# Performance work log

Measured on AMD Instinct MI355X. Metric: run time of the kernel, lower is better.

The kernel has to match this reference:

```python
import jax, jax.numpy as jnp
import numpy as np

N_NODES = 100_000
N_EDGES = 1_600_000
IN_FEATS = 64
H_DIMS = 64
OUT_A = 2
OUT_B = 21
N_LAYERS = 2
EPS = 1e-5


def setup_inputs() -> dict:
    key = jax.random.key(0)
    ks = jax.random.split(key, 16)
    d = H_DIMS

    def rn(k, shape, scale=0.05):
        return jax.random.normal(k, shape, dtype=jnp.float32) * scale

    return {
        "v": jax.random.normal(ks[0], (N_NODES, IN_FEATS), dtype=jnp.float32),
        "src": jax.random.randint(ks[1], (N_EDGES,), 0, N_NODES),
        "dst": jax.random.randint(ks[2], (N_EDGES,), 0, N_NODES),
        "rel_type": jax.random.randint(ks[3], (N_EDGES,), 0, 3),
        "norm": jax.random.uniform(ks[4], (N_EDGES,), dtype=jnp.float32),
        "emb_W": rn(ks[5], (d, IN_FEATS)),
        "emb_b": jnp.zeros((d,), jnp.float32),
        "emb_gamma": jnp.ones((d,), jnp.float32),
        "emb_beta": jnp.zeros((d,), jnp.float32),
        "rel_weight": rn(ks[6], (3, d, d)),
        "gru_Wih": rn(ks[7], (3 * d, d)),
        "gru_Whh": rn(ks[8], (3 * d, d)),
        "gru_bih": jnp.zeros((3 * d,), jnp.float32),
        "gru_bhh": jnp.zeros((3 * d,), jnp.float32),
        "ker_gamma": jnp.ones((d,), jnp.float32),
        "ker_beta": jnp.zeros((d,), jnp.float32),
        "a_W1": rn(ks[9], (d, d)), "a_b1": jnp.zeros((d,), jnp.float32),
        "a_gamma": jnp.ones((d,), jnp.float32), "a_beta": jnp.zeros((d,), jnp.float32),
        "a_W2": rn(ks[10], (OUT_A, d)), "a_b2": jnp.zeros((OUT_A,), jnp.float32),
        "b_W1": rn(ks[11], (d, d)), "b_b1": jnp.zeros((d,), jnp.float32),
        "b_gamma": jnp.ones((d,), jnp.float32), "b_beta": jnp.zeros((d,), jnp.float32),
        "b_W2": rn(ks[12], (OUT_B, d)), "b_b2": jnp.zeros((OUT_B,), jnp.float32),
    }


def _bn(x, gamma, beta):
    # BatchNorm1d in training mode: batch statistics, biased variance
    mu = jnp.mean(x, axis=0)
    var = jnp.var(x, axis=0)
    return (x - mu) * jax.lax.rsqrt(var + EPS) * gamma + beta


def _gru_cell(x, h, Wih, Whh, bih, bhh):
    # torch nn.GRU single layer, gate order (r, z, n)
    gi = x @ Wih.T + bih
    gh = h @ Whh.T + bhh
    ir, iz, inn = jnp.split(gi, 3, axis=-1)
    hr, hz, hn = jnp.split(gh, 3, axis=-1)
    r = jax.nn.sigmoid(ir + hr)
    z = jax.nn.sigmoid(iz + hz)
    n = jnp.tanh(inn + r * hn)
    return (1.0 - z) * n + z * h


def reference(v, src, dst, rel_type, norm, emb_W, emb_b, emb_gamma, emb_beta,
              rel_weight, gru_Wih, gru_Whh, gru_bih, gru_bhh, ker_gamma, ker_beta,
              a_W1, a_b1, a_gamma, a_beta, a_W2, a_b2,
              b_W1, b_b1, b_gamma, b_beta, b_W2, b_b2):
    # Embedding: Linear -> BN -> ReLU
    h0 = jax.nn.relu(_bn(v @ emb_W.T + emb_b, emb_gamma, emb_beta))
    output = h0
    h = jnp.zeros_like(h0)
    n_nodes = v.shape[0]
    for _ in range(N_LAYERS):
        # per-node relational transform for all 3 relations: [N, 3, d]
        x3 = jnp.einsum('nd,rdk->nrk', output, rel_weight)
        msg = x3[src, rel_type] * norm[:, None]                     # [E, d]
        swh = jax.ops.segment_sum(msg, dst, num_segments=n_nodes)   # [N, d]
        h = _gru_cell(swh, h, gru_Wih, gru_Whh, gru_bih, gru_bhh)
        output = h
    hk = _bn(output, ker_gamma, ker_beta)
    # task heads: Linear -> BN -> ReLU -> Linear (MLP with h_layers=2)
    xa = jax.nn.relu(_bn(hk @ a_W1.T + a_b1, a_gamma, a_beta)) @ a_W2.T + a_b2
    xb = jax.nn.relu(_bn(hk @ b_W1.T + b_b1, b_gamma, b_beta)) @ b_W2.T + b_b2
    return xa, xb
```

## Files before the change

### kernel.cpp

```cpp
#include <hip/hip_runtime.h>

#define NN 100000
#define NE 1600000
#define NP 100096
#define NBKT 391
#define CAP 6144
#define EPSV 1e-5f

typedef unsigned int u32;
typedef unsigned short u16;
typedef unsigned long long u64;
typedef __bf16 bf16x8 __attribute__((ext_vector_type(8)));
typedef float f32x4 __attribute__((ext_vector_type(4)));

#define GLBP(x) ((const __attribute__((address_space(1))) u32*)(x))
#define LDSP(x) ((__attribute__((address_space(3))) u32*)(x))

__device__ __forceinline__ u16 f2bf(float f) {
  u32 x = __float_as_uint(f);
  return (u16)((x + 0x7FFFu + ((x >> 16) & 1u)) >> 16);
}
__device__ __forceinline__ float bf2f(u16 h) { return __uint_as_float(((u32)h) << 16); }

__device__ __forceinline__ void pack_one(const float* W, u32* out, int K, int KOT, int i) {
  int q = i & 3, lane = (i >> 2) & 63, f = i >> 8;
  int ks = f / KOT, ot = f - ks * KOT;
  int o = ot * 16 + (lane & 15);
  int k = ks * 32 + (lane >> 4) * 8 + q * 2;
  out[i] = (u32)f2bf(W[o * K + k]) | ((u32)f2bf(W[o * K + k + 1]) << 16);
}

__global__ void setupA(const float* __restrict__ relw, const float* __restrict__ Wih,
                       const float* __restrict__ embW, const float* __restrict__ Whh,
                       float* __restrict__ Wrow, u32* __restrict__ PWem, u32* __restrict__ PWhh) {
  int b = blockIdx.x;
  if (b < 144) {
    int t = b * 256 + threadIdx.x;
    if (t >= 192 * 192) return;
    int kg = t / 192, j = t % 192;
    const float* a = relw + (j >> 6) * 4096 + (j & 63) * 64;
    const float* w = Wih + kg * 64;
    float s = 0.f;
#pragma unroll
    for (int k = 0; k < 64; ++k) s += a[k] * w[k];
    Wrow[kg * 192 + j] = s;
  } else if (b < 152) {
    pack_one(embW, PWem, 64, 4, (b - 144) * 256 + threadIdx.x);
  } else {
    pack_one(Whh, PWhh, 64, 12, (b - 152) * 256 + threadIdx.x);
  }
}

__global__ void pack_wf(const float* __restrict__ Wrow, u32* __restrict__ PWf) {
  pack_one(Wrow, PWf, 192, 12, blockIdx.x * 256 + threadIdx.x);
}

__global__ void fold_pack(const float* __restrict__ Wa, const float* __restrict__ Wb,
                          const float* __restrict__ sc, u32* __restrict__ Pa,
                          u32* __restrict__ Pb) {
  int iu = blockIdx.x * 256 + threadIdx.x;
  int hsel = iu >> 11;
  int i = iu & 2047;
  const float* W = hsel ? Wb : Wa;
  u32* P = hsel ? Pb : Pa;
  int q = i & 3, lane = (i >> 2) & 63, f = i >> 8;
  int ks = f >> 2, ot = f & 3;
  int o = ot * 16 + (lane & 15);
  int k = ks * 32 + (lane >> 4) * 8 + q * 2;
  P[i] = (u32)f2bf(W[o * 64 + k] * sc[k]) | ((u32)f2bf(W[o * 64 + k + 1] * sc[k + 1]) << 16);
}

__global__ __launch_bounds__(256) void countplace(const int* __restrict__ src,
                                                  const int* __restrict__ dst,
                                                  const int* __restrict__ rt,
                                                  const float* __restrict__ nrm,
                                                  int* __restrict__ gcnt,
                                                  u64* __restrict__ region) {
  __shared__ u32 hist[NBKT], gbase[NBKT];
  const int t = threadIdx.x;
  for (int i = t; i < NBKT; i += 256) hist[i] = 0;
  __syncthreads();
  const int e0 = blockIdx.x * 2048 + t;
  u32 rlo[8], rhi[8], lrank[8];
  int bkt[8];
#pragma unroll
  for (int i = 0; i < 8; ++i) {
    int e = e0 + i * 256;
    bkt[i] = -1;
    if (e < NE) {
      int d = dst[e];
      int b = d >> 8;
      bkt[i] = b;
      lrank[i] = atomicAdd(&hist[b], 1u);
      rlo[i] = (u32)src[e] | ((u32)rt[e] << 20) | ((u32)(d & 255) << 22);
      rhi[i] = __float_as_uint(nrm[e]);
    }
  }
  __syncthreads();
  for (int i = t; i < NBKT; i += 256) {
    u32 h = hist[i];
    gbase[i] = h ? (u32)atomicAdd(&gcnt[i], (int)h) : 0u;
  }
  __syncthreads();
#pragma unroll
  for (int i = 0; i < 8; ++i) {
    if (bkt[i] >= 0) {
      u32 pos = gbase[bkt[i]] + lrank[i];
      if (pos < CAP)
        region[(size_t)bkt[i] * CAP + pos] = (u64)rlo[i] | ((u64)rhi[i] << 32);
    }
  }
}

__global__ __launch_bounds__(512) void bucketscan(const int* __restrict__ gcnt,
                                                  int* __restrict__ bbase,
                                                  int* __restrict__ rowp) {
  int t = threadIdx.x;
  int v = (t < NBKT) ? gcnt[t] : 0;
  __shared__ int sh[512];
  sh[t] = v;
  __syncthreads();
#pragma unroll
  for (int off = 1; off < 512; off <<= 1) {
    int u = (t >= off) ? sh[t - off] : 0;
    __syncthreads();
    sh[t] += u;
    __syncthreads();
  }
  if (t < NBKT) bbase[t] = sh[t] - v;
  if (t == 0) rowp[NN] = NE;
}

__global__ __launch_bounds__(256) void localsort(const int* __restrict__ gcnt,
                                                 const int* __restrict__ bbase,
                                                 const u64* __restrict__ region,
                                                 u64* __restrict__ csr,
                                                 int* __restrict__ rowp) {
  const int b = blockIdx.x, t = threadIdx.x;
  int n = gcnt[b];
  if (n > CAP) n = CAP;
  const int base = bbase[b];
  __shared__ u32 hist[256], sc[256];
  hist[t] = 0;
  __syncthreads();
  for (int i = t; i < n; i += 256)
    atomicAdd(&hist[((u32)region[(size_t)b * CAP + i] >> 22) & 255], 1u);
  __syncthreads();
  u32 v = hist[t];
  sc[t] = v;
  __syncthreads();
#pragma unroll
  for (int off = 1; off < 256; off <<= 1) {
    u32 u = (t >= off) ? sc[t - off] : 0;
    __syncthreads();
    sc[t] += u;
    __syncthreads();
  }
  u32 excl = sc[t] - v;
  int node = b * 256 + t;
  if (node < NN) rowp[node] = base + (int)excl;
  __syncthreads();
  hist[t] = excl;
  __syncthreads();
  for (int i = t; i < n; i += 256) {
    u64 rec = region[(size_t)b * CAP + i];
    u32 pos = atomicAdd(&hist[((u32)rec >> 22) & 255], 1u);
    csr[(size_t)base + pos] = rec;
  }
}

__global__ __launch_bounds__(256) void csr_gather(const int* __restrict__ rowp,
                                                  const u64* __restrict__ csr,
                                                  const u16* __restrict__ Xbf,
                                                  u16* __restrict__ ACCbf) {
  int wv = blockIdx.x * 4 + (threadIdx.x >> 6);
  int lane = threadIdx.x & 63;
  if (wv >= NN) return;
  const int half = lane >> 5, c2 = lane & 31;
  int base = rowp[wv], end = rowp[wv + 1];
  float a0x = 0.f, a0y = 0.f, a1x = 0.f, a1y = 0.f, a2x = 0.f, a2y = 0.f;
#define GP(JJ)                                                                   \
  { u32 sA = (u32)__builtin_amdgcn_readlane((int)lo, (JJ));                      \
    u32 sB = (u32)__builtin_amdgcn_readlane((int)lo, (JJ) + 1);                  \
    u32 nA = (u32)__builtin_amdgcn_readlane((int)hi, (JJ));                      \
    u32 nB = (u32)__builtin_amdgcn_readlane((int)hi, (JJ) + 1);                  \
    u32 srp = half ? sB : sA;                                                    \
    float nm = __uint_as_float(half ? nB : nA);                                  \
    u32 xw = *(const u32*)(Xbf + (size_t)(srp & 0xFFFFFu) * 64 + 2 * c2);        \
    float x0 = bf2f((u16)xw), x1 = bf2f((u16)(xw >> 16));                        \
    int r = (int)((srp >> 20) & 3);                                              \
    float n0 = (r == 0) ? nm : 0.f;                                              \
    float n1 = (r == 1) ? nm : 0.f;                                              \
    float n2 = (r == 2) ? nm : 0.f;                                              \
    a0x = fmaf(x0, n0, a0x); a0y = fmaf(x1, n0, a0y);                            \
    a1x = fmaf(x0, n1, a1x); a1y = fmaf(x1, n1, a1y);                            \
    a2x = fmaf(x0, n2, a2x); a2y = fmaf(x1, n2, a2y); }
  for (int c = base; c < end; c += 64) {
    int m = end - c; m = m > 64 ? 64 : m;
    u32 lo = 0, hi = 0;
    if (lane < m) {
      u64 r = csr[(size_t)c + lane];
      lo = (u32)r; hi = (u32)(r >> 32);
    }
    int j = 0;
    for (; j + 16 <= m; j += 16) {
      GP(j) GP(j + 2) GP(j + 4) GP(j + 6)
      GP(j + 8) GP(j + 10) GP(j + 12) GP(j + 14)
    }
    for (; j < m; j += 2) { GP(j) }
  }
#undef GP
  a0x += __shfl_xor(a0x, 32); a0y += __shfl_xor(a0y, 32);
  a1x += __shfl_xor(a1x, 32); a1y += __shfl_xor(a1y, 32);
  a2x += __shfl_xor(a2x, 32); a2y += __shfl_xor(a2y, 32);
  if (half == 0) {
    u32* orow = (u32*)(ACCbf + (size_t)wv * 192);
    orow[c2]      = (u32)f2bf(a0x) | ((u32)f2bf(a0y) << 16);
    orow[32 + c2] = (u32)f2bf(a1x) | ((u32)f2bf(a1y) << 16);
    orow[64 + c2] = (u32)f2bf(a2x) | ((u32)f2bf(a2y) << 16);
  }
}

template<int K, int KO, int AF32, int GRU, int CS, int OUTBF>
__global__ __launch_bounds__(256) void gemm_mfma(
    const void* __restrict__ Av, const u32* __restrict__ Wpk, void* __restrict__ Yv,
    const float* __restrict__ bih, const float* __restrict__ bhh,
    const u16* __restrict__ G2B, const u16* __restrict__ Hv,
    float* __restrict__ csum, int n) {
  constexpr int KOT = KO / 16, KS = K / 32;
  constexpr int NFRAG = KS * KOT;
  __shared__ u32 bsh[NFRAG * 256];
  __shared__ float cs[128];
  const int lane = threadIdx.x & 63, w = threadIdx.x >> 6;
  const int rr = lane & 15, kg = lane >> 4;
  const long mbase = (long)blockIdx.x * 128 + w * 32;
  const u16* Abf = (const u16*)Av;
  const float* Af = (const float*)Av;

  auto loadAbf = [&](int ks, int halfsel) -> bf16x8 {
    if (AF32) {
      long r = mbase + halfsel * 16 + rr;
      if (r > n - 1) r = n - 1;
      const float* pp = Af + r * K + ks * 32 + kg * 8;
      float4 u0 = *(const float4*)pp;
      float4 u1 = *(const float4*)(pp + 4);
      bf16x8 o_;
      o_[0] = __builtin_bit_cast(__bf16, f2bf(u0.x));
      o_[1] = __builtin_bit_cast(__bf16, f2bf(u0.y));
      o_[2] = __builtin_bit_cast(__bf16, f2bf(u0.z));
      o_[3] = __builtin_bit_cast(__bf16, f2bf(u0.w));
      o_[4] = __builtin_bit_cast(__bf16, f2bf(u1.x));
      o_[5] = __builtin_bit_cast(__bf16, f2bf(u1.y));
      o_[6] = __builtin_bit_cast(__bf16, f2bf(u1.z));
      o_[7] = __builtin_bit_cast(__bf16, f2bf(u1.w));
      return o_;
    }
    return *reinterpret_cast<const bf16x8*>(Abf + (mbase + halfsel * 16 + rr) * K + ks * 32 + kg * 8);
  };

  constexpr int PASSES = NFRAG / 4;
#pragma unroll
  for (int i = 0; i < PASSES; ++i) {
    int c = i * 4 + w;
    __builtin_amdgcn_global_load_lds(GLBP(Wpk + (long)c * 256 + lane * 4),
                                     LDSP(&bsh[c * 256]), 16, 0, 0);
  }
  bf16x8 a0 = loadAbf(0, 0);
  bf16x8 a1 = loadAbf(0, 1);
  __syncthreads();

  f32x4 acc[2][KOT] = {};
#pragma unroll
  for (int ks = 0; ks < KS; ++ks) {
    bf16x8 c0 = a0, c1 = a1;
    if (ks + 1 < KS) {
      a0 = loadAbf(ks + 1, 0);
      a1 = loadAbf(ks + 1, 1);
    }
#pragma unroll
    for (int o = 0; o < KOT; ++o) {
      bf16x8 bfr = *reinterpret_cast<const bf16x8*>(&bsh[((ks * KOT + o) * 64 + lane) * 4]);
      acc[0][o] = __builtin_amdgcn_mfma_f32_16x16x32_bf16(c0, bfr, acc[0][o], 0, 0, 0);
      acc[1][o] = __builtin_amdgcn_mfma_f32_16x16x32_bf16(c1, bfr, acc[1][o], 0, 0, 0);
    }
  }

  float s[4] = {0.f, 0.f, 0.f, 0.f}, ss[4] = {0.f, 0.f, 0.f, 0.f};
  if (GRU == 0) {
#pragma unroll
    for (int tl = 0; tl < 2; ++tl)
#pragma unroll
      for (int o = 0; o < KOT; ++o)
#pragma unroll
        for (int q = 0; q < 4; ++q) {
          long row = mbase + tl * 16 + kg * 4 + q;
          float vv = acc[tl][o][q];
          if (row < n) {
            long off = row * KO + o * 16 + rr;
            if (OUTBF) ((u16*)Yv)[off] = f2bf(vv);
            else       ((float*)Yv)[off] = vv;
            if (CS) { s[o & 3] += vv; ss[o & 3] += vv * vv; }
          }
        }
  } else {
    float bi[12], bh_[12];
#pragma unroll
    for (int g = 0; g < 3; ++g)
#pragma unroll
      for (int o = 0; o < 4; ++o) {
        bi[g * 4 + o] = bih[g * 64 + o * 16 + rr];
        bh_[g * 4 + o] = bhh[g * 64 + o * 16 + rr];
      }
#pragma unroll
    for (int tl = 0; tl < 2; ++tl)
#pragma unroll
      for (int o = 0; o < 4; ++o) {
        int c = o * 16 + rr;
#pragma unroll
        for (int q = 0; q < 4; ++q) {
          long row = mbase + tl * 16 + kg * 4 + q;
          float ir = acc[tl][o][q] + bi[o];
          float iz = acc[tl][o + 4][q] + bi[4 + o];
          float in_ = acc[tl][o + 8][q] + bi[8 + o];
          float hr = bh_[o], hz = bh_[4 + o], hn = bh_[8 + o], hv = 0.f;
          if (GRU == 2) {
            const u16* g2 = G2B + row * 192;
            hr += bf2f(g2[c]); hz += bf2f(g2[64 + c]); hn += bf2f(g2[128 + c]);
            hv = bf2f(Hv[row * 64 + c]);
          }
          float rg = 1.f / (1.f + __expf(-(ir + hr)));
          float zg = 1.f / (1.f + __expf(-(iz + hz)));
          float ng = tanhf(in_ + rg * hn);
          float h = (1.f - zg) * ng + (GRU == 2 ? zg * hv : 0.f);
          if (row < n) {
            ((u16*)Yv)[row * 64 + c] = f2bf(h);
            if (CS) { s[o] += h; ss[o] += h * h; }
          }
        }
      }
  }
  if (CS) {
    for (int i = threadIdx.x; i < 128; i += 256) cs[i] = 0.f;
    __syncthreads();
#pragma unroll
    for (int o = 0; o < 4; ++o) {
      int c = o * 16 + rr;
      atomicAdd(&cs[c], s[o]);
      atomicAdd(&cs[64 + c], ss[o]);
    }
    __syncthreads();
    if (threadIdx.x < 128) atomicAdd(&csum[threadIdx.x], cs[threadIdx.x]);
  }
}

__global__ void bn_finalize(const float* __restrict__ acc, const float* __restrict__ gamma,
                            const float* __restrict__ beta, float* __restrict__ scsh,
                            float inv_n) {
  int t = threadIdx.x;
  float mean = acc[t] * inv_n;
  float var = acc[64 + t] * inv_n - mean * mean;
  float sc = gamma[t] * rsqrtf(var + EPSV);
  scsh[t] = sc;
  scsh[64 + t] = beta[t] - mean * sc;
}

__global__ __launch_bounds__(256) void bn_apply_bf(const float* __restrict__ X,
                                                   u16* __restrict__ Y,
                                                   const float* __restrict__ scsh, int relu) {
  long i = (long)blockIdx.x * 256 + threadIdx.x;
  float4 v = reinterpret_cast<const float4*>(X)[i];
  int c = (int)((i * 4) & 63);
  v.x = fmaf(v.x, scsh[c],     scsh[64 + c]);
  v.y = fmaf(v.y, scsh[c + 1], scsh[65 + c]);
  v.z = fmaf(v.z, scsh[c + 2], scsh[66 + c]);
  v.w = fmaf(v.w, scsh[c + 3], scsh[67 + c]);
  if (relu) {
    v.x = fmaxf(v.x, 0.f); v.y = fmaxf(v.y, 0.f);
    v.z = fmaxf(v.z, 0.f); v.w = fmaxf(v.w, 0.f);
  }
  reinterpret_cast<ushort4*>(Y)[i] = make_ushort4(f2bf(v.x), f2bf(v.y), f2bf(v.z), f2bf(v.w));
}

template<int KO>
__global__ __launch_bounds__(256) void headfin_bn(const float* __restrict__ Z,
                                                  const float* __restrict__ scsh,
                                                  const float* __restrict__ W2,
                                                  const float* __restrict__ b2,
                                                  float* __restrict__ out, int n) {
  __shared__ float ws[KO * 64];
  for (int i = threadIdx.x; i < KO * 64; i += 256) ws[i] = W2[i];
  __syncthreads();
  long node = (long)blockIdx.x * 256 + threadIdx.x;
  if (node >= n) return;
  float x[64];
#pragma unroll
  for (int i = 0; i < 16; ++i) {
    float4 z4 = reinterpret_cast<const float4*>(Z + node * 64)[i];
    int c = i * 4;
    x[c]     = fmaxf(fmaf(z4.x, scsh[c],     scsh[64 + c]), 0.f);
    x[c + 1] = fmaxf(fmaf(z4.y, scsh[c + 1], scsh[65 + c]), 0.f);
    x[c + 2] = fmaxf(fmaf(z4.z, scsh[c + 2], scsh[66 + c]), 0.f);
    x[c + 3] = fmaxf(fmaf(z4.w, scsh[c + 3], scsh[67 + c]), 0.f);
  }
#pragma unroll
  for (int o = 0; o < KO; ++o) {
    float a = b2[o];
#pragma unroll
    for (int d = 0; d < 64; ++d) a = fmaf(x[d], ws[o * 64 + d], a);
    out[node * KO + o] = a;
  }
}

extern "C" void kernel_launch(void* const* d_in, const int* in_sizes, int n_in,
                              void* d_out, int out_size, void* d_ws, size_t ws_size,
                              hipStream_t stream) {
  const float* v     = (const float*)d_in[0];
  const int*   src   = (const int*)d_in[1];
  const int*   dst   = (const int*)d_in[2];
  const int*   rt    = (const int*)d_in[3];
  const float* norm  = (const float*)d_in[4];
  const float* emb_W = (const float*)d_in[5];
  const float* emb_g  = (const float*)d_in[7];
  const float* emb_be = (const float*)d_in[8];
  const float* rel_w  = (const float*)d_in[9];
  const float* Wih    = (const float*)d_in[10];
  const float* Whh    = (const float*)d_in[11];
  const float* bih    = (const float*)d_in[12];
  const float* bhh    = (const float*)d_in[13];
  const float* ker_g  = (const float*)d_in[14];
  const float* ker_be = (const float*)d_in[15];
  const float* aW1    = (const float*)d_in[16];
  const float* a_g  = (const float*)d_in[18];
  const float* a_be = (const float*)d_in[19];
  const float* aW2  = (const float*)d_in[20];
  const float* ab2  = (const float*)d_in[21];
  const float* bW1  = (const float*)d_in[22];
  const float* b_g  = (const float*)d_in[24];
  const float* b_be = (const float*)d_in[25];
  const float* bW2  = (const float*)d_in[26];
  const float* bb2  = (const float*)d_in[27];
  float* out = (float*)d_out;

  char* p = (char*)d_ws;
  auto nxt = [&](size_t bytes) -> char* {
    char* r = p; p += (bytes + 255) & ~(size_t)255; return r;
  };
  int*   GCNT = (int*)nxt(512 * 4);
  float* ACCs = (float*)nxt(512 * 4);
  float* Z    = (float*)nxt((size_t)NP * 64 * 4);
  u16*   X1   = (u16*)nxt((size_t)NP * 64 * 2);
  u16*   X2   = (u16*)nxt((size_t)NP * 64 * 2);
  u16*   ACCB = (u16*)nxt((size_t)NP * 192 * 2);
  u16*   G2B  = (u16*)nxt((size_t)NP * 192 * 2);
  u64*   REG  = (u64*)nxt((size_t)NBKT * CAP * 8);
  u64*   CSR  = (u64*)nxt((size_t)NE * 8);
  int*   BBAS = (int*)nxt(512 * 4);
  int*   ROWP = (int*)nxt((size_t)(NN + 8) * 4);
  u32*   PWf  = (u32*)nxt(18432 * 4);
  u32*   PWem = (u32*)nxt(2048 * 4);
  u32*   PWhh = (u32*)nxt(6144 * 4);
  u32*   PWa  = (u32*)nxt(2048 * 4);
  u32*   PWb  = (u32*)nxt(2048 * 4);
  float* WROW = (float*)nxt(147456);
  float* SC   = (float*)nxt(512 * 4);

  hipMemsetAsync(GCNT, 0, 1024 * 4, stream);

  setupA<<<176, 256, 0, stream>>>(rel_w, Wih, emb_W, Whh, WROW, PWem, PWhh);
  countplace<<<782, 256, 0, stream>>>(src, dst, rt, norm, GCNT, REG);
  bucketscan<<<1, 512, 0, stream>>>(GCNT, BBAS, ROWP);
  localsort<<<NBKT, 256, 0, stream>>>(GCNT, BBAS, REG, CSR, ROWP);
  pack_wf<<<72, 256, 0, stream>>>(WROW, PWf);

  gemm_mfma<64, 64, 1, 0, 1, 0><<<782, 256, 0, stream>>>(v, PWem, Z, nullptr, nullptr,
                                                         nullptr, nullptr, ACCs + 0, NN);
  bn_finalize<<<1, 64, 0, stream>>>(ACCs + 0, emb_g, emb_be, SC + 0, 1.f / NN);
  bn_apply_bf<<<6250, 256, 0, stream>>>(Z, X2, SC + 0, 1);

  csr_gather<<<25000, 256, 0, stream>>>(ROWP, CSR, X2, ACCB);
  gemm_mfma<192, 192, 0, 1, 0, 1><<<782, 256, 0, stream>>>(ACCB, PWf, X1, bih, bhh,
                                                           nullptr, nullptr, nullptr, NN);

  csr_gather<<<25000, 256, 0, stream>>>(ROWP, CSR, X1, ACCB);
  gemm_mfma<64, 192, 0, 0, 0, 1><<<782, 256, 0, stream>>>(X1, PWhh, G2B, nullptr, nullptr,
                                                          nullptr, nullptr, nullptr, NN);
  gemm_mfma<192, 192, 0, 2, 1, 1><<<782, 256, 0, stream>>>(ACCB, PWf, X1, bih, bhh,
                                                           G2B, X1, ACCs + 128, NN);

  bn_finalize<<<1, 64, 0, stream>>>(ACCs + 128, ker_g, ker_be, SC + 128, 1.f / NN);
  fold_pack<<<16, 256, 0, stream>>>(aW1, bW1, SC + 128, PWa, PWb);

  gemm_mfma<64, 64, 0, 0, 1, 0><<<782, 256, 0, stream>>>(X1, PWa, Z, nullptr, nullptr,
                                                         nullptr, nullptr, ACCs + 256, NN);
  bn_finalize<<<1, 64, 0, stream>>>(ACCs + 256, a_g, a_be, SC + 256, 1.f / NN);
  headfin_bn<2><<<391, 256, 0, stream>>>(Z, SC + 256, aW2, ab2, out, NN);

  gemm_mfma<64, 64, 0, 0, 1, 0><<<782, 256, 0, stream>>>(X1, PWb, Z, nullptr, nullptr,
                                                         nullptr, nullptr, ACCs + 384, NN);
  bn_finalize<<<1, 64, 0, stream>>>(ACCs + 384, b_g, b_be, SC + 384, 1.f / NN);
  headfin_bn<21><<<391, 256, 0, stream>>>(Z, SC + 384, bW2, bb2, out + (long)NN * 2, NN);
}
```

Measured before the change: 419.1 us.

## Split CSR by relation, fuse head GEMMs, and fold BN finalize into consumers

localsort now sorts by node and relation together, so each node gets four row pointers and csr_gather builds three separate per-relation accumulators instead of three masked FMAs per edge. The two head first-layer GEMMs are merged into one 128-wide GEMM that writes a bf16 intermediate. The bn_finalize launches are removed and their work is recomputed inside bn_apply_bf, headfin_bn and fold_pack. This cuts gather ALU work, kernel launches and intermediate traffic, at the cost of more rowptr memory, bf16 rounding of the head pre-activations, and possibly more divergent per-relation loops.

New measurement: 414.2 us. No clear change (-1.2%).

```diff
diff --git a/kernel.cpp b/kernel.cpp
--- a/kernel.cpp
+++ b/kernel.cpp
@@ -56,18 +56,20 @@
 }
 
 __global__ void fold_pack(const float* __restrict__ Wa, const float* __restrict__ Wb,
-                          const float* __restrict__ sc, u32* __restrict__ Pa,
-                          u32* __restrict__ Pb) {
-  int iu = blockIdx.x * 256 + threadIdx.x;
-  int hsel = iu >> 11;
-  int i = iu & 2047;
-  const float* W = hsel ? Wb : Wa;
-  u32* P = hsel ? Pb : Pa;
+                          const float* __restrict__ kacc, const float* __restrict__ kg,
+                          u32* __restrict__ P) {
+  int i = blockIdx.x * 256 + threadIdx.x;
   int q = i & 3, lane = (i >> 2) & 63, f = i >> 8;
-  int ks = f >> 2, ot = f & 3;
+  int ks = f >> 3, ot = f & 7;
   int o = ot * 16 + (lane & 15);
   int k = ks * 32 + (lane >> 4) * 8 + q * 2;
-  P[i] = (u32)f2bf(W[o * 64 + k] * sc[k]) | ((u32)f2bf(W[o * 64 + k + 1] * sc[k + 1]) << 16);
+  const float* W = (o < 64) ? (Wa + o * 64) : (Wb + (o - 64) * 64);
+  const float inv = 1.f / NN;
+  float m0 = kacc[k] * inv;
+  float s0 = kg[k] * rsqrtf(kacc[64 + k] * inv - m0 * m0 + EPSV);
+  float m1 = kacc[k + 1] * inv;
+  float s1 = kg[k + 1] * rsqrtf(kacc[64 + k + 1] * inv - m1 * m1 + EPSV);
+  P[i] = (u32)f2bf(W[k] * s0) | ((u32)f2bf(W[k + 1] * s1) << 16);
 }
 
 __global__ __launch_bounds__(256) void countplace(const int* __restrict__ src,
@@ -113,8 +115,7 @@
 }
 
 __global__ __launch_bounds__(512) void bucketscan(const int* __restrict__ gcnt,
-                                                  int* __restrict__ bbase,
-                                                  int* __restrict__ rowp) {
+                                                  int* __restrict__ bbase) {
   int t = threadIdx.x;
   int v = (t < NBKT) ? gcnt[t] : 0;
   __shared__ int sh[512];
@@ -128,26 +129,27 @@
     __syncthreads();
   }
   if (t < NBKT) bbase[t] = sh[t] - v;
-  if (t == 0) rowp[NN] = NE;
 }
 
 __global__ __launch_bounds__(256) void localsort(const int* __restrict__ gcnt,
                                                  const int* __restrict__ bbase,
                                                  const u64* __restrict__ region,
                                                  u64* __restrict__ csr,
-                                                 int* __restrict__ rowp) {
+                                                 int* __restrict__ rowpr) {
   const int b = blockIdx.x, t = threadIdx.x;
   int n = gcnt[b];
   if (n > CAP) n = CAP;
   const int base = bbase[b];
-  __shared__ u32 hist[256], sc[256];
-  hist[t] = 0;
+  __shared__ u32 hist[1024], sc[256];
+#pragma unroll
+  for (int i = 0; i < 4; ++i) hist[t + 256 * i] = 0;
   __syncthreads();
   for (int i = t; i < n; i += 256)
-    atomicAdd(&hist[((u32)region[(size_t)b * CAP + i] >> 22) & 255], 1u);
-  __syncthreads();
-  u32 v = hist[t];
-  sc[t] = v;
+    atomicAdd(&hist[(u32)(region[(size_t)b * CAP + i] >> 20) & 1023u], 1u);
+  __syncthreads();
+  u32 a0 = hist[4 * t], a1 = hist[4 * t + 1], a2 = hist[4 * t + 2], a3 = hist[4 * t + 3];
+  u32 part = a0 + a1 + a2 + a3;
+  sc[t] = part;
   __syncthreads();
 #pragma unroll
   for (int off = 1; off < 256; off <<= 1) {
@@ -156,20 +158,24 @@
     sc[t] += u;
     __syncthreads();
   }
-  u32 excl = sc[t] - v;
+  u32 ex = sc[t] - part;
   int node = b * 256 + t;
-  if (node < NN) rowp[node] = base + (int)excl;
-  __syncthreads();
-  hist[t] = excl;
+  rowpr[4 * node + 0] = base + (int)ex;
+  rowpr[4 * node + 1] = base + (int)(ex + a0);
+  rowpr[4 * node + 2] = base + (int)(ex + a0 + a1);
+  rowpr[4 * node + 3] = base + (int)(ex + a0 + a1 + a2);
+  __syncthreads();
+  hist[4 * t] = ex; hist[4 * t + 1] = ex + a0;
+  hist[4 * t + 2] = ex + a0 + a1; hist[4 * t + 3] = ex + a0 + a1 + a2;
   __syncthreads();
   for (int i = t; i < n; i += 256) {
     u64 rec = region[(size_t)b * CAP + i];
-    u32 pos = atomicAdd(&hist[((u32)rec >> 22) & 255], 1u);
+    u32 pos = atomicAdd(&hist[(u32)(rec >> 20) & 1023u], 1u);
     csr[(size_t)base + pos] = rec;
   }
 }
 
-__global__ __launch_bounds__(256) void csr_gather(const int* __restrict__ rowp,
+__global__ __launch_bounds__(256) void csr_gather(const int* __restrict__ rowpr,
                                                   const u64* __restrict__ csr,
                                                   const u16* __restrict__ Xbf,
                                                   u16* __restrict__ ACCbf) {
@@ -177,48 +183,47 @@
   int lane = threadIdx.x & 63;
   if (wv >= NN) return;
   const int half = lane >> 5, c2 = lane & 31;
-  int base = rowp[wv], end = rowp[wv + 1];
-  float a0x = 0.f, a0y = 0.f, a1x = 0.f, a1y = 0.f, a2x = 0.f, a2y = 0.f;
-#define GP(JJ)                                                                   \
-  { u32 sA = (u32)__builtin_amdgcn_readlane((int)lo, (JJ));                      \
-    u32 sB = (u32)__builtin_amdgcn_readlane((int)lo, (JJ) + 1);                  \
-    u32 nA = (u32)__builtin_amdgcn_readlane((int)hi, (JJ));                      \
-    u32 nB = (u32)__builtin_amdgcn_readlane((int)hi, (JJ) + 1);                  \
-    u32 srp = half ? sB : sA;                                                    \
-    float nm = __uint_as_float(half ? nB : nA);                                  \
-    u32 xw = *(const u32*)(Xbf + (size_t)(srp & 0xFFFFFu) * 64 + 2 * c2);        \
-    float x0 = bf2f((u16)xw), x1 = bf2f((u16)(xw >> 16));                        \
-    int r = (int)((srp >> 20) & 3);                                              \
-    float n0 = (r == 0) ? nm : 0.f;                                              \
-    float n1 = (r == 1) ? nm : 0.f;                                              \
-    float n2 = (r == 2) ? nm : 0.f;                                              \
-    a0x = fmaf(x0, n0, a0x); a0y = fmaf(x1, n0, a0y);                            \
-    a1x = fmaf(x0, n1, a1x); a1y = fmaf(x1, n1, a1y);                            \
-    a2x = fmaf(x0, n2, a2x); a2y = fmaf(x1, n2, a2y); }
-  for (int c = base; c < end; c += 64) {
-    int m = end - c; m = m > 64 ? 64 : m;
-    u32 lo = 0, hi = 0;
-    if (lane < m) {
-      u64 r = csr[(size_t)c + lane];
-      lo = (u32)r; hi = (u32)(r >> 32);
-    }
-    int j = 0;
-    for (; j + 16 <= m; j += 16) {
-      GP(j) GP(j + 2) GP(j + 4) GP(j + 6)
-      GP(j + 8) GP(j + 10) GP(j + 12) GP(j + 14)
-    }
-    for (; j < m; j += 2) { GP(j) }
-  }
-#undef GP
-  a0x += __shfl_xor(a0x, 32); a0y += __shfl_xor(a0y, 32);
-  a1x += __shfl_xor(a1x, 32); a1y += __shfl_xor(a1y, 32);
-  a2x += __shfl_xor(a2x, 32); a2y += __shfl_xor(a2y, 32);
-  if (half == 0) {
-    u32* orow = (u32*)(ACCbf + (size_t)wv * 192);
-    orow[c2]      = (u32)f2bf(a0x) | ((u32)f2bf(a0y) << 16);
-    orow[32 + c2] = (u32)f2bf(a1x) | ((u32)f2bf(a1y) << 16);
-    orow[64 + c2] = (u32)f2bf(a2x) | ((u32)f2bf(a2y) << 16);
-  }
+  int4 rp = *reinterpret_cast<const int4*>(rowpr + 4 * wv);
+  const int bnd[4] = {rp.x, rp.y, rp.z, rp.w};
+  u32* orow = (u32*)(ACCbf + (size_t)wv * 192);
+#define PAIRF(J)                                                                  \
+  { u32 sA = (u32)__builtin_amdgcn_readlane((int)lo, (J));                        \
+    u32 sB = (u32)__builtin_amdgcn_readlane((int)lo, (J) + 1);                    \
+    u32 nA = (u32)__builtin_amdgcn_readlane((int)hi, (J));                        \
+    u32 nB = (u32)__builtin_amdgcn_readlane((int)hi, (J) + 1);                    \
+    u32 srp = half ? sB : sA;                                                     \
+    float nm = __uint_as_float(half ? nB : nA);                                   \
+    u32 xw = *(const u32*)(Xbf + (size_t)(srp & 0xFFFFFu) * 64 + 2 * c2);         \
+    ax = fmaf(__uint_as_float(xw << 16), nm, ax);                                 \
+    ay = fmaf(__uint_as_float(xw & 0xFFFF0000u), nm, ay); }
+#pragma unroll
+  for (int r = 0; r < 3; ++r) {
+    int b0 = bnd[r], e0 = bnd[r + 1];
+    float ax = 0.f, ay = 0.f;
+    for (int c = b0; c < e0; c += 64) {
+      int m = e0 - c; m = m > 64 ? 64 : m;
+      u32 lo = 0, hi = 0;
+      if (lane < m) {
+        u64 rec = csr[(size_t)c + lane];
+        lo = (u32)rec; hi = (u32)(rec >> 32);
+      }
+      int j = 0;
+      for (; j + 4 <= m; j += 4) { PAIRF(j) PAIRF(j + 2) }
+      for (; j + 2 <= m; j += 2) { PAIRF(j) }
+      if (j < m) {
+        u32 sA = (u32)__builtin_amdgcn_readlane((int)lo, j);
+        u32 nA = (u32)__builtin_amdgcn_readlane((int)hi, j);
+        float nm = __uint_as_float(half ? 0u : nA);
+        u32 xw = *(const u32*)(Xbf + (size_t)(sA & 0xFFFFFu) * 64 + 2 * c2);
+        ax = fmaf(__uint_as_float(xw << 16), nm, ax);
+        ay = fmaf(__uint_as_float(xw & 0xFFFF0000u), nm, ay);
+      }
+    }
+    ax += __shfl_xor(ax, 32);
+    ay += __shfl_xor(ay, 32);
+    if (half == 0) orow[r * 32 + c2] = (u32)f2bf(ax) | ((u32)f2bf(ay) << 16);
+  }
+#undef PAIRF
 }
 
 template<int K, int KO, int AF32, int GRU, int CS, int OUTBF>
@@ -230,7 +235,7 @@
   constexpr int KOT = KO / 16, KS = K / 32;
   constexpr int NFRAG = KS * KOT;
   __shared__ u32 bsh[NFRAG * 256];
-  __shared__ float cs[128];
+  __shared__ float cs[2 * KO];
   const int lane = threadIdx.x & 63, w = threadIdx.x >> 6;
   const int rr = lane & 15, kg = lane >> 4;
   const long mbase = (long)blockIdx.x * 128 + w * 32;
@@ -285,7 +290,7 @@
     }
   }
 
-  float s[4] = {0.f, 0.f, 0.f, 0.f}, ss[4] = {0.f, 0.f, 0.f, 0.f};
+  float s[KOT] = {}, ss[KOT] = {};
   if (GRU == 0) {
 #pragma unroll
     for (int tl = 0; tl < 2; ++tl)
@@ -299,7 +304,7 @@
             long off = row * KO + o * 16 + rr;
             if (OUTBF) ((u16*)Yv)[off] = f2bf(vv);
             else       ((float*)Yv)[off] = vv;
-            if (CS) { s[o & 3] += vv; ss[o & 3] += vv * vv; }
+            if (CS) { s[o] += vv; ss[o] += vv * vv; }
           }
         }
   } else {
@@ -340,34 +345,38 @@
       }
   }
   if (CS) {
-    for (int i = threadIdx.x; i < 128; i += 256) cs[i] = 0.f;
+    constexpr int LIM = (GRU == 0) ? 2 * KO : 128;
+    constexpr int CKO = (GRU == 0) ? KO : 64;
+    constexpr int OL = (GRU == 0) ? KOT : 4;
+    for (int i = threadIdx.x; i < LIM; i += 256) cs[i] = 0.f;
     __syncthreads();
 #pragma unroll
-    for (int o = 0; o < 4; ++o) {
+    for (int o = 0; o < OL; ++o) {
       int c = o * 16 + rr;
       atomicAdd(&cs[c], s[o]);
-      atomicAdd(&cs[64 + c], ss[o]);
+      atomicAdd(&cs[CKO + c], ss[o]);
     }
     __syncthreads();
-    if (threadIdx.x < 128) atomicAdd(&csum[threadIdx.x], cs[threadIdx.x]);
-  }
-}
-
-__global__ void bn_finalize(const float* __restrict__ acc, const float* __restrict__ gamma,
-                            const float* __restrict__ beta, float* __restrict__ scsh,
-                            float inv_n) {
-  int t = threadIdx.x;
-  float mean = acc[t] * inv_n;
-  float var = acc[64 + t] * inv_n - mean * mean;
-  float sc = gamma[t] * rsqrtf(var + EPSV);
-  scsh[t] = sc;
-  scsh[64 + t] = beta[t] - mean * sc;
+    for (int i = threadIdx.x; i < LIM; i += 256) atomicAdd(&csum[i], cs[i]);
+  }
 }
 
 __global__ __launch_bounds__(256) void bn_apply_bf(const float* __restrict__ X,
                                                    u16* __restrict__ Y,
-                                                   const float* __restrict__ scsh, int relu) {
-  long i = (long)blockIdx.x * 256 + threadIdx.x;
+                                                   const float* __restrict__ accs,
+                                                   const float* __restrict__ gamma,
+                                                   const float* __restrict__ beta, int relu) {
+  __shared__ float scsh[128];
+  int t = threadIdx.x;
+  if (t < 64) {
+    float mean = accs[t] * (1.f / NN);
+    float var = accs[64 + t] * (1.f / NN) - mean * mean;
+    float sc = gamma[t] * rsqrtf(var + EPSV);
+    scsh[t] = sc;
+    scsh[64 + t] = beta[t] - mean * sc;
+  }
+  __syncthreads();
+  long i = (long)blockIdx.x * 256 + t;
   float4 v = reinterpret_cast<const float4*>(X)[i];
   int c = (int)((i * 4) & 63);
   v.x = fmaf(v.x, scsh[c],     scsh[64 + c]);
@@ -382,25 +391,38 @@
 }
 
 template<int KO>
-__global__ __launch_bounds__(256) void headfin_bn(const float* __restrict__ Z,
-                                                  const float* __restrict__ scsh,
+__global__ __launch_bounds__(256) void headfin_bn(const u16* __restrict__ Z,
+                                                  const float* __restrict__ asum,
+                                                  const float* __restrict__ asq,
+                                                  const float* __restrict__ gamma,
+                                                  const float* __restrict__ beta,
                                                   const float* __restrict__ W2,
                                                   const float* __restrict__ b2,
                                                   float* __restrict__ out, int n) {
   __shared__ float ws[KO * 64];
-  for (int i = threadIdx.x; i < KO * 64; i += 256) ws[i] = W2[i];
-  __syncthreads();
-  long node = (long)blockIdx.x * 256 + threadIdx.x;
+  __shared__ float scsh[128];
+  int t = threadIdx.x;
+  if (t < 64) {
+    float mean = asum[t] * (1.f / NN);
+    float var = asq[t] * (1.f / NN) - mean * mean;
+    float sc = gamma[t] * rsqrtf(var + EPSV);
+    scsh[t] = sc;
+    scsh[64 + t] = beta[t] - mean * sc;
+  }
+  for (int i = t; i < KO * 64; i += 256) ws[i] = W2[i];
+  __syncthreads();
+  long node = (long)blockIdx.x * 256 + t;
   if (node >= n) return;
+  const u16* zr = Z + node * 128;
   float x[64];
 #pragma unroll
   for (int i = 0; i < 16; ++i) {
-    float4 z4 = reinterpret_cast<const float4*>(Z + node * 64)[i];
+    ushort4 z4 = reinterpret_cast<const ushort4*>(zr)[i];
     int c = i * 4;
-    x[c]     = fmaxf(fmaf(z4.x, scsh[c],     scsh[64 + c]), 0.f);
-    x[c + 1] = fmaxf(fmaf(z4.y, scsh[c + 1], scsh[65 + c]), 0.f);
-    x[c + 2] = fmaxf(fmaf(z4.z, scsh[c + 2], scsh[66 + c]), 0.f);
-    x[c + 3] = fmaxf(fmaf(z4.w, scsh[c + 3], scsh[67 + c]), 0.f);
+    x[c]     = fmaxf(fmaf(bf2f(z4.x), scsh[c],     scsh[64 + c]), 0.f);
+    x[c + 1] = fmaxf(fmaf(bf2f(z4.y), scsh[c + 1], scsh[65 + c]), 0.f);
+    x[c + 2] = fmaxf(fmaf(bf2f(z4.z), scsh[c + 2], scsh[66 + c]), 0.f);
+    x[c + 3] = fmaxf(fmaf(bf2f(z4.w), scsh[c + 3], scsh[67 + c]), 0.f);
   }
 #pragma unroll
   for (int o = 0; o < KO; ++o) {
@@ -428,7 +450,6 @@
   const float* bih    = (const float*)d_in[12];
   const float* bhh    = (const float*)d_in[13];
   const float* ker_g  = (const float*)d_in[14];
-  const float* ker_be = (const float*)d_in[15];
   const float* aW1    = (const float*)d_in[16];
   const float* a_g  = (const float*)d_in[18];
   const float* a_be = (const float*)d_in[19];
@@ -455,48 +476,40 @@
   u64*   REG  = (u64*)nxt((size_t)NBKT * CAP * 8);
   u64*   CSR  = (u64*)nxt((size_t)NE * 8);
   int*   BBAS = (int*)nxt(512 * 4);
-  int*   ROWP = (int*)nxt((size_t)(NN + 8) * 4);
+  int*   ROWPR = (int*)nxt((size_t)(NP + 8) * 4 * 4);
   u32*   PWf  = (u32*)nxt(18432 * 4);
   u32*   PWem = (u32*)nxt(2048 * 4);
   u32*   PWhh = (u32*)nxt(6144 * 4);
-  u32*   PWa  = (u32*)nxt(2048 * 4);
-  u32*   PWb  = (u32*)nxt(2048 * 4);
+  u32*   PWab = (u32*)nxt(4096 * 4);
   float* WROW = (float*)nxt(147456);
-  float* SC   = (float*)nxt(512 * 4);
 
   hipMemsetAsync(GCNT, 0, 1024 * 4, stream);
 
   setupA<<<176, 256, 0, stream>>>(rel_w, Wih, emb_W, Whh, WROW, PWem, PWhh);
   countplace<<<782, 256, 0, stream>>>(src, dst, rt, norm, GCNT, REG);
-  bucketscan<<<1, 512, 0, stream>>>(GCNT, BBAS, ROWP);
-  localsort<<<NBKT, 256, 0, stream>>>(GCNT, BBAS, REG, CSR, ROWP);
+  bucketscan<<<1, 512, 0, stream>>>(GCNT, BBAS);
+  localsort<<<NBKT, 256, 0, stream>>>(GCNT, BBAS, REG, CSR, ROWPR);
   pack_wf<<<72, 256, 0, stream>>>(WROW, PWf);
 
   gemm_mfma<64, 64, 1, 0, 1, 0><<<782, 256, 0, stream>>>(v, PWem, Z, nullptr, nullptr,
                                                          nullptr, nullptr, ACCs + 0, NN);
-  bn_finalize<<<1, 64, 0, stream>>>(ACCs + 0, emb_g, emb_be, SC + 0, 1.f / NN);
-  bn_apply_bf<<<6250, 256, 0, stream>>>(Z, X2, SC + 0, 1);
-
-  csr_gather<<<25000, 256, 0, stream>>>(ROWP, CSR, X2, ACCB);
+  bn_apply_bf<<<6250, 256, 0, stream>>>(Z, X2, ACCs + 0, emb_g, emb_be, 1);
+
+  csr_gather<<<25000, 256, 0, stream>>>(ROWPR, CSR, X2, ACCB);
   gemm_mfma<192, 192, 0, 1, 0, 1><<<782, 256, 0, stream>>>(ACCB, PWf, X1, bih, bhh,
                                                            nullptr, nullptr, nullptr, NN);
 
-  csr_gather<<<25000, 256, 0, stream>>>(ROWP, CSR, X1, ACCB);
+  csr_gather<<<25000, 256, 0, stream>>>(ROWPR, CSR, X1, ACCB);
   gemm_mfma<64, 192, 0, 0, 0, 1><<<782, 256, 0, stream>>>(X1, PWhh, G2B, nullptr, nullptr,
                                                           nullptr, nullptr, nullptr, NN);
   gemm_mfma<192, 192, 0, 2, 1, 1><<<782, 256, 0, stream>>>(ACCB, PWf, X1, bih, bhh,
                                                            G2B, X1, ACCs + 128, NN);
 
-  bn_finalize<<<1, 64, 0, stream>>>(ACCs + 128, ker_g, ker_be, SC + 128, 1.f / NN);
-  fold_pack<<<16, 256, 0, stream>>>(aW1, bW1, SC + 128, PWa, PWb);
-
-  gemm_mfma<64, 64, 0, 0, 1, 0><<<782, 256, 0, stream>>>(X1, PWa, Z, nullptr, nullptr,
-                                                         nullptr, nullptr, ACCs + 256, NN);
-  bn_finalize<<<1, 64, 0, stream>>>(ACCs + 256, a_g, a_be, SC + 256, 1.f / NN);
-  headfin_bn<2><<<391, 256, 0, stream>>>(Z, SC + 256, aW2, ab2, out, NN);
-
-  gemm_mfma<64, 64, 0, 0, 1, 0><<<782, 256, 0, stream>>>(X1, PWb, Z, nullptr, nullptr,
-                                                         nullptr, nullptr, ACCs + 384, NN);
-  bn_finalize<<<1, 64, 0, stream>>>(ACCs + 384, b_g, b_be, SC + 384, 1.f / NN);
-  headfin_bn<21><<<391, 256, 0, stream>>>(Z, SC + 384, bW2, bb2, out + (long)NN * 2, NN);
-}
+  fold_pack<<<16, 256, 0, stream>>>(aW1, bW1, ACCs + 128, ker_g, PWab);
+  gemm_mfma<64, 128, 0, 0, 1, 1><<<782, 256, 0, stream>>>(X1, PWab, ACCB, nullptr, nullptr,
+                                                          nullptr, nullptr, ACCs + 256, NN);
+  headfin_bn<2><<<391, 256, 0, stream>>>((const u16*)ACCB, ACCs + 256, ACCs + 384,
+                                         a_g, a_be, aW2, ab2, out, NN);
+  headfin_bn<21><<<391, 256, 0, stream>>>((const u16*)ACCB + 64, ACCs + 320, ACCs + 448,
+                                          b_g, b_be, bW2, bb2, out + (long)NN * 2, NN);
+}
```
